# Kernel tuning notes

Measured on AMD Instinct MI355X. Metric: run time of the kernel, lower is better.

## Reference

```python
import jax, jax.numpy as jnp
import numpy as np

B, T, DIM, H = 4, 2048, 512, 8
DECAY = 0.9

def setup_inputs():
    key = jax.random.key(0)
    ks = jax.random.split(key, 8)
    s = 1.0 / np.sqrt(DIM)
    def lin(k):
        return jax.random.normal(k, (DIM, DIM), jnp.float32) * s
    return {
        "q": jax.random.normal(ks[0], (B, T, DIM), jnp.float32),
        "k": jax.random.normal(ks[1], (B, T, DIM), jnp.float32),
        "v": jax.random.normal(ks[2], (B, T, DIM), jnp.float32),
        "Wa": lin(ks[3]), "ba": jnp.zeros((DIM,), jnp.float32),
        "Wb": lin(ks[4]), "bb": jnp.zeros((DIM,), jnp.float32),
        "Wg": lin(ks[5]), "bg": jnp.zeros((DIM,), jnp.float32),
        "Wo": lin(ks[6]), "bo": jnp.zeros((DIM,), jnp.float32),
    }

def _linear_scan(a, b):
    # h_t = a_t * h_{t-1} + b_t along time axis=1, via associative scan
    def combine(c1, c2):
        a1, b1 = c1
        a2, b2 = c2
        return a1 * a2, a2 * b1 + b2
    return jax.lax.associative_scan(combine, (a, b), axis=1)[1]

def reference(q, k, v, Wa, ba, Wb, bb, Wg, bg, Wo, bo):
    # --- Mamba-style selective scan on q (no residual) ---
    a = jax.nn.sigmoid(q @ Wa + ba)   # input-dependent decay [B,T,D]
    b = q @ Wb + bb                   # input injection       [B,T,D]
    h = _linear_scan(a, b)            # recurrent state       [B,T,D]
    g = jax.nn.sigmoid(q @ Wg + bg)   # gate
    m_out = (h * g) @ Wo + bo         # [B,T,D]

    # --- RetNet-style decay-weighted linear retention ---
    Dh = DIM // H
    qh = q.reshape(B, T, H, Dh)
    kh = k.reshape(B, T, H, Dh)
    vh = v.reshape(B, T, H, Dh)
    t = jnp.arange(T)
    delta = t[:, None] - t[None, :]           # t - s
    mask = delta >= 0                         # causal
    decay_mat = jnp.where(
        mask,
        jnp.exp(jnp.where(mask, delta, 0).astype(jnp.float32) * np.float32(np.log(DECAY))),
        0.0,
    )                                          # [T,T]
    scores = jnp.einsum('bthd,bshd->bhts', qh, kh) * decay_mat  # [B,H,T,T]
    r_out = jnp.einsum('bhts,bshd->bthd', scores, vh).reshape(B, T, DIM)

    return m_out + r_out
```

## Files before the change

### kernel.cpp

```cpp
#include <hip/hip_runtime.h>
#include <hip/hip_bf16.h>

typedef unsigned short u16;

#define BB 4
#define TT 2048
#define DIM 512
#define NH 8
#define DH 64
#define DECAY 0.9f

#define CC 64
#define NC 32
#define BHN 32

#define CHS 32
#define NSC 64

#define TM 128
#define TN 128
#define BK 64

#define SS 72

typedef __attribute__((ext_vector_type(8))) short bf16x8;
typedef __attribute__((ext_vector_type(4))) float f32x4;

__device__ __forceinline__ u16 f2bfu(float f) {
  union { float f; unsigned int u; } c; c.f = f;
  unsigned int u = c.u + 0x7FFFu + ((c.u >> 16) & 1u);
  return (u16)(u >> 16);
}
__device__ __forceinline__ float bf2f(u16 u) {
  union { unsigned int u; float f; } c; c.u = ((unsigned int)u) << 16;
  return c.f;
}

__device__ __forceinline__ void gl_lds16(const void* g, void* l) {
  __builtin_amdgcn_global_load_lds(
      (const __attribute__((address_space(1))) void*)g,
      (__attribute__((address_space(3))) void*)(unsigned int)(unsigned long long)l,
      16, 0, 0);
}

__device__ __forceinline__ void gemm_tile(
    int nTile, int mTile, const u16* __restrict__ A, const u16* __restrict__ Bt,
    const float* __restrict__ b0, const float* __restrict__ b1,
    const float* __restrict__ b2,
    u16* __restrict__ C0, u16* __restrict__ C1, u16* __restrict__ C2,
    int act_mask, u16* As, u16* Bs, int tid) {
  int wave = tid >> 6, lane = tid & 63;
  int group = (nTile * TN) >> 9;
  const float* bias = (group == 0) ? b0 : (group == 1) ? b1 : b2;
  u16* C = (group == 0) ? C0 : (group == 1) ? C1 : C2;
  int act = (act_mask >> group) & 1;

  int wm = (wave >> 1) * 64, wn = (wave & 1) * 64;
  int rowA = lane & 15, khalf = lane >> 4;

  f32x4 acc[4][4];
#pragma unroll
  for (int i = 0; i < 4; ++i)
#pragma unroll
    for (int j = 0; j < 4; ++j) acc[i][j] = (f32x4){0.f, 0.f, 0.f, 0.f};

  const u16* Abase = A + (size_t)mTile * TM * 512;
  const u16* Bbase = Bt + (size_t)nTile * TN * 512;

  for (int kk = 0; kk < 512; kk += BK) {
#pragma unroll
    for (int i = 0; i < 4; ++i) {
      int o = (wave * 4 + i) * 64 + lane;
      int row = o >> 3, gk = (o & 7) ^ (row & 7);
      gl_lds16(Abase + (size_t)row * 512 + kk + gk * 8, &As[o * 8]);
    }
#pragma unroll
    for (int i = 0; i < 4; ++i) {
      int o = (wave * 4 + i) * 64 + lane;
      int row = o >> 3, gk = (o & 7) ^ (row & 7);
      gl_lds16(Bbase + (size_t)row * 512 + kk + gk * 8, &Bs[o * 8]);
    }
    __syncthreads();
#pragma unroll
    for (int k0 = 0; k0 < 2; ++k0) {
      bf16x8 af[4], bfr[4];
#pragma unroll
      for (int mi = 0; mi < 4; ++mi) {
        int rr = wm + mi * 16 + rowA;
        int gk = k0 * 4 + khalf;
        int o = rr * 8 + (gk ^ (rr & 7));
        af[mi] = *(const bf16x8*)&As[o * 8];
      }
#pragma unroll
      for (int ni = 0; ni < 4; ++ni) {
        int rr = wn + ni * 16 + rowA;
        int gk = k0 * 4 + khalf;
        int o = rr * 8 + (gk ^ (rr & 7));
        bfr[ni] = *(const bf16x8*)&Bs[o * 8];
      }
#pragma unroll
      for (int mi = 0; mi < 4; ++mi)
#pragma unroll
        for (int ni = 0; ni < 4; ++ni)
          acc[mi][ni] = __builtin_amdgcn_mfma_f32_16x16x32_bf16(
              af[mi], bfr[ni], acc[mi][ni], 0, 0, 0);
    }
    __syncthreads();
  }
  int cloc = lane & 15, rq = (lane >> 4) * 4;
#pragma unroll
  for (int mi = 0; mi < 4; ++mi) {
#pragma unroll
    for (int r = 0; r < 4; ++r) {
      int m = mTile * TM + wm + mi * 16 + rq + r;
#pragma unroll
      for (int ni = 0; ni < 4; ++ni) {
        int n = (nTile * TN + wn + ni * 16 + cloc) & 511;
        float vv = acc[mi][ni][r] + bias[n];
        if (act) vv = 1.0f / (1.0f + __expf(-vv));
        C[(size_t)m * 512 + n] = f2bfu(vv);
      }
    }
  }
}

__device__ __forceinline__ void gemm_tile64(
    int nTile, int mTile, const u16* __restrict__ A, const u16* __restrict__ Bt,
    const float* __restrict__ bias, float* __restrict__ C,
    const u16* __restrict__ Radd, u16* As, u16* Bs, int tid) {
  int wave = tid >> 6, lane = tid & 63;
  int wm = wave * 32;
  int rowA = lane & 15, khalf = lane >> 4;

  f32x4 acc[2][4];
#pragma unroll
  for (int i = 0; i < 2; ++i)
#pragma unroll
    for (int j = 0; j < 4; ++j) acc[i][j] = (f32x4){0.f, 0.f, 0.f, 0.f};

  const u16* Abase = A + (size_t)mTile * TM * 512;
  const u16* Bbase = Bt + (size_t)nTile * 64 * 512;

  for (int kk = 0; kk < 512; kk += BK) {
#pragma unroll
    for (int i = 0; i < 4; ++i) {
      int o = (wave * 4 + i) * 64 + lane;
      int row = o >> 3, gk = (o & 7) ^ (row & 7);
      gl_lds16(Abase + (size_t)row * 512 + kk + gk * 8, &As[o * 8]);
    }
#pragma unroll
    for (int i = 0; i < 2; ++i) {
      int o = (wave * 2 + i) * 64 + lane;
      int row = o >> 3, gk = (o & 7) ^ (row & 7);
      gl_lds16(Bbase + (size_t)row * 512 + kk + gk * 8, &Bs[o * 8]);
    }
    __syncthreads();
#pragma unroll
    for (int k0 = 0; k0 < 2; ++k0) {
      bf16x8 af[2], bfr[4];
#pragma unroll
      for (int mi = 0; mi < 2; ++mi) {
        int rr = wm + mi * 16 + rowA;
        int gk = k0 * 4 + khalf;
        int o = rr * 8 + (gk ^ (rr & 7));
        af[mi] = *(const bf16x8*)&As[o * 8];
      }
#pragma unroll
      for (int ni = 0; ni < 4; ++ni) {
        int rr = ni * 16 + rowA;
        int gk = k0 * 4 + khalf;
        int o = rr * 8 + (gk ^ (rr & 7));
        bfr[ni] = *(const bf16x8*)&Bs[o * 8];
      }
#pragma unroll
      for (int mi = 0; mi < 2; ++mi)
#pragma unroll
        for (int ni = 0; ni < 4; ++ni)
          acc[mi][ni] = __builtin_amdgcn_mfma_f32_16x16x32_bf16(
              af[mi], bfr[ni], acc[mi][ni], 0, 0, 0);
    }
    __syncthreads();
  }
  int cloc = lane & 15, rq = (lane >> 4) * 4;
#pragma unroll
  for (int mi = 0; mi < 2; ++mi) {
#pragma unroll
    for (int r = 0; r < 4; ++r) {
      int m = mTile * TM + wm + mi * 16 + rq + r;
#pragma unroll
      for (int ni = 0; ni < 4; ++ni) {
        int n = nTile * 64 + ni * 16 + cloc;
        float vv = acc[mi][ni][r] + bias[n] + bf2f(Radd[(size_t)m * 512 + n]);
        C[(size_t)m * 512 + n] = vv;
      }
    }
  }
}

__global__ __launch_bounds__(256) void k1_prep_retkv(
    const float* __restrict__ q, u16* __restrict__ qbf,
    const float* __restrict__ W0, const float* __restrict__ W1,
    const float* __restrict__ W2, const float* __restrict__ W3,
    u16* __restrict__ Wt,
    const float* __restrict__ k, const float* __restrict__ v,
    u16* __restrict__ KVTb, u16* __restrict__ VTg) {
  __shared__ __align__(16) u16 smem[2 * 64 * SS];
  __shared__ float t[32][33];
  int bx = blockIdx.x, tid = threadIdx.x;
  if (bx < 1024) {
    int bh = bx & 31, c = bx >> 5;
    int b = bh >> 3, h = bh & 7;
    int wave = tid >> 6, lane = tid & 63;
    u16* VT = smem;
    u16* KT = smem + 64 * SS;
    size_t base = ((size_t)(b * TT + c * CC)) * DIM + h * DH;
    int row = tid >> 2, part = tid & 3, e0 = part * 16;
    float w = __powf(DECAY, (float)(63 - row));
    {
      const float4* vs = (const float4*)(v + base + (size_t)row * DIM + e0);
      const float4* ks = (const float4*)(k + base + (size_t)row * DIM + e0);
#pragma unroll
      for (int u4 = 0; u4 < 4; ++u4) {
        float4 fv = vs[u4], fk = ks[u4];
        VT[(e0 + u4 * 4 + 0) * SS + row] = f2bfu(fv.x);
        VT[(e0 + u4 * 4 + 1) * SS + row] = f2bfu(fv.y);
        VT[(e0 + u4 * 4 + 2) * SS + row] = f2bfu(fv.z);
        VT[(e0 + u4 * 4 + 3) * SS + row] = f2bfu(fv.w);
        KT[(e0 + u4 * 4 + 0) * SS + row] = f2bfu(fk.x * w);
        KT[(e0 + u4 * 4 + 1) * SS + row] = f2bfu(fk.y * w);
        KT[(e0 + u4 * 4 + 2) * SS + row] = f2bfu(fk.z * w);
        KT[(e0 + u4 * 4 + 3) * SS + row] = f2bfu(fk.w * w);
      }
    }
    __syncthreads();
    {
      int e = row;
      u16* dst = VTg + ((size_t)bh * 64 + e) * TT + c * 64 + part * 16;
      *(uint4*)dst = *(const uint4*)&VT[e * SS + part * 16];
      *(uint4*)(dst + 8) = *(const uint4*)&VT[e * SS + part * 16 + 8];
    }
    int wm = (wave >> 1) * 32, wn = (wave & 1) * 32;
    int rowA = lane & 15, khalf = lane >> 4;
    f32x4 acc[2][2];
#pragma unroll
    for (int i = 0; i < 2; ++i)
#pragma unroll
      for (int j = 0; j < 2; ++j) acc[i][j] = (f32x4){0.f, 0.f, 0.f, 0.f};
#pragma unroll
    for (int k0 = 0; k0 < 2; ++k0) {
      int gk = k0 * 4 + khalf;
      bf16x8 af[2], bfr[2];
#pragma unroll
      for (int mi = 0; mi < 2; ++mi)
        af[mi] = *(const bf16x8*)&VT[(wm + mi * 16 + rowA) * SS + gk * 8];
#pragma unroll
      for (int ni = 0; ni < 2; ++ni)
        bfr[ni] = *(const bf16x8*)&KT[(wn + ni * 16 + rowA) * SS + gk * 8];
#pragma unroll
      for (int mi = 0; mi < 2; ++mi)
#pragma unroll
        for (int ni = 0; ni < 2; ++ni)
          acc[mi][ni] = __builtin_amdgcn_mfma_f32_16x16x32_bf16(
              af[mi], bfr[ni], acc[mi][ni], 0, 0, 0);
    }
    int cloc = lane & 15, rq = (lane >> 4) * 4;
    u16* o = KVTb + ((size_t)(c * BHN + bh)) * 4096;
#pragma unroll
    for (int mi = 0; mi < 2; ++mi)
#pragma unroll
      for (int r = 0; r < 4; ++r) {
        int e = wm + mi * 16 + rq + r;
#pragma unroll
        for (int ni = 0; ni < 2; ++ni)
          o[e * 64 + (wn + ni * 16 + cloc)] = f2bfu(acc[mi][ni][r]);
      }
  } else if (bx < 2048) {
    int bx2 = bx - 1024;
    int m = bx2 >> 8, rem = bx2 & 255;
    int n0 = (rem & 15) * 32, k0 = (rem >> 4) * 32;
    const float* W = (m == 0) ? W0 : (m == 1) ? W1 : (m == 2) ? W2 : W3;
    int tx = tid & 31, ty = tid >> 5;
#pragma unroll
    for (int r = 0; r < 32; r += 8)
      t[ty + r][tx] = W[(size_t)(k0 + ty + r) * DIM + n0 + tx];
    __syncthreads();
    u16* o = Wt + (size_t)m * DIM * DIM;
#pragma unroll
    for (int r = 0; r < 32; r += 8)
      o[(size_t)(n0 + ty + r) * DIM + k0 + tx] = f2bfu(t[tx][ty + r]);
  } else {
    int i = (bx - 2048) * 256 + tid;
    float4 f = ((const float4*)q)[i];
    ushort4 u;
    u.x = f2bfu(f.x); u.y = f2bfu(f.y); u.z = f2bfu(f.z); u.w = f2bfu(f.w);
    ((ushort4*)qbf)[i] = u;
  }
}

__global__ __launch_bounds__(256) void k2_gemm1_retscan(
    const u16* __restrict__ qbf, const u16* __restrict__ WtAll,
    const float* __restrict__ ba, const float* __restrict__ bb,
    const float* __restrict__ bg,
    u16* __restrict__ Ab16, u16* __restrict__ Bb16, u16* __restrict__ Gb16,
    const u16* __restrict__ KVTb, u16* __restrict__ Ptb) {
  __shared__ __align__(16) u16 smem[TM * BK + TN * BK];
  int bx = blockIdx.x, tid = threadIdx.x;
  if (bx < 768) {
    int r = bx & 7, t6 = bx >> 3;
    int nT = t6 % 12, s = t6 / 12;
    int mT = (s << 3) | r;
    gemm_tile(nT, mT, qbf, WtAll, ba, bb, bg, Ab16, Bb16, Gb16,
              0b101, smem, smem + TM * BK, tid);
  } else {
    int gid = (bx - 768) * 256 + tid;
    int bh = gid >> 12, ed = gid & 4095;
    float carry = 0.f;
    const float dC = __powf(DECAY, (float)CC);
    for (int c = 0; c < NC; ++c) {
      size_t idx = ((size_t)(c * BHN + bh)) * 4096 + ed;
      Ptb[idx] = f2bfu(carry);
      carry = fmaf(dC, carry, bf2f(KVTb[idx]));
    }
  }
}

__global__ void k3_part(const u16* __restrict__ Ab16, const u16* __restrict__ Bb16,
                        float* __restrict__ SA, float* __restrict__ SB) {
  int ci = blockIdx.x >> 3, grp = blockIdx.x & 7;
  int ch = grp * 256 + threadIdx.x;
  int bb2 = ch >> 9, d = ch & 511;
  size_t base = ((size_t)bb2 * TT + ci * CHS) * DIM + d;
  float h = 0.f, pA = 1.f;
#pragma unroll
  for (int t = 0; t < CHS; ++t) {
    float av = bf2f(Ab16[base + (size_t)t * DIM]);
    float bv = bf2f(Bb16[base + (size_t)t * DIM]);
    h = fmaf(av, h, bv);
    pA *= av;
  }
  SA[ci * 2048 + ch] = pA;
  SB[ci * 2048 + ch] = h;
}

__global__ __launch_bounds__(256) void k4_apply_retout(
    const u16* __restrict__ Ab16, const u16* __restrict__ Bb16,
    const u16* __restrict__ g, const float* __restrict__ SA,
    const float* __restrict__ SB, u16* __restrict__ hg,
    const u16* __restrict__ qbf, const float* __restrict__ kg,
    const u16* __restrict__ VTg, const u16* __restrict__ Ptb,
    u16* __restrict__ routb) {
  __shared__ __align__(16) u16 Sa[64 * SS];
  __shared__ float dp[66];
  int bx = blockIdx.x, tid = threadIdx.x;
  if (bx < 512) {
    int ci = bx >> 3, grp = bx & 7;
    int ch = grp * 256 + tid;
    int bb = ch >> 9, d = ch & 511;
    float carry = 0.f;
    for (int p = 0; p < ci; ++p)
      carry = fmaf(SA[p * 2048 + ch], carry, SB[p * 2048 + ch]);
    size_t base = ((size_t)bb * TT + ci * CHS) * DIM + d;
    float h = carry;
#pragma unroll
    for (int t = 0; t < CHS; ++t) {
      size_t idx = base + (size_t)t * DIM;
      h = fmaf(bf2f(Ab16[idx]), h, bf2f(Bb16[idx]));
      hg[idx] = f2bfu(h * bf2f(g[idx]));
    }
    return;
  }
  int idx2 = bx - 512;
  int bh = idx2 & 31, c = idx2 >> 5;
  int b = bh >> 3, h = bh & 7;
  int wave = tid >> 6, lane = tid & 63;
  size_t base = ((size_t)(b * TT + c * CC)) * DIM + h * DH;
  if (tid < 66) dp[tid] = __powf(DECAY, (float)tid);

  int wm = (wave >> 1) * 32, wn = (wave & 1) * 32;
  int rowA = lane & 15, khalf = lane >> 4;

  bf16x8 afq[2][2];
#pragma unroll
  for (int k0 = 0; k0 < 2; ++k0)
#pragma unroll
    for (int mi = 0; mi < 2; ++mi)
      afq[k0][mi] = *(const bf16x8*)(qbf + base +
          (size_t)(wm + mi * 16 + rowA) * 512 + (k0 * 4 + khalf) * 8);
  bf16x8 bfk[2][2];
#pragma unroll
  for (int k0 = 0; k0 < 2; ++k0)
#pragma unroll
    for (int ni = 0; ni < 2; ++ni) {
      const float* kp = kg + base + (size_t)(wn + ni * 16 + rowA) * 512 +
                        (k0 * 4 + khalf) * 8;
      float4 f0 = *(const float4*)kp;
      float4 f1 = *(const float4*)(kp + 4);
      bf16x8 t;
      t[0] = (short)f2bfu(f0.x); t[1] = (short)f2bfu(f0.y);
      t[2] = (short)f2bfu(f0.z); t[3] = (short)f2bfu(f0.w);
      t[4] = (short)f2bfu(f1.x); t[5] = (short)f2bfu(f1.y);
      t[6] = (short)f2bfu(f1.z); t[7] = (short)f2bfu(f1.w);
      bfk[k0][ni] = t;
    }

  f32x4 accS[2][2];
#pragma unroll
  for (int i = 0; i < 2; ++i)
#pragma unroll
    for (int j = 0; j < 2; ++j) accS[i][j] = (f32x4){0.f, 0.f, 0.f, 0.f};
#pragma unroll
  for (int k0 = 0; k0 < 2; ++k0)
#pragma unroll
    for (int mi = 0; mi < 2; ++mi)
#pragma unroll
      for (int ni = 0; ni < 2; ++ni)
        accS[mi][ni] = __builtin_amdgcn_mfma_f32_16x16x32_bf16(
            afq[k0][mi], bfk[k0][ni], accS[mi][ni], 0, 0, 0);
  __syncthreads();

  int cloc = lane & 15, rq = (lane >> 4) * 4;
#pragma unroll
  for (int mi = 0; mi < 2; ++mi)
#pragma unroll
    for (int ni = 0; ni < 2; ++ni)
#pragma unroll
      for (int r = 0; r < 4; ++r) {
        int i = wm + mi * 16 + rq + r;
        int j = wn + ni * 16 + cloc;
        float sv = (j <= i) ? accS[mi][ni][r] * dp[i - j] : 0.f;
        Sa[i * SS + j] = f2bfu(sv);
      }
#pragma unroll
  for (int mi = 0; mi < 2; ++mi) {
    float s = dp[wm + mi * 16 + rowA + 1];
#pragma unroll
    for (int k0 = 0; k0 < 2; ++k0) {
      bf16x8 t = afq[k0][mi];
#pragma unroll
      for (int u = 0; u < 8; ++u)
        t[u] = (short)f2bfu(bf2f((u16)t[u]) * s);
      afq[k0][mi] = t;
    }
  }
  __syncthreads();

  f32x4 accO[2][2];
#pragma unroll
  for (int i = 0; i < 2; ++i)
#pragma unroll
    for (int j = 0; j < 2; ++j) accO[i][j] = (f32x4){0.f, 0.f, 0.f, 0.f};
#pragma unroll
  for (int k0 = 0; k0 < 4; ++k0) {
    bf16x8 af[2], bfv[2];
#pragma unroll
    for (int mi = 0; mi < 2; ++mi) {
      if (k0 < 2)
        af[mi] = *(const bf16x8*)&Sa[(wm + mi * 16 + rowA) * SS +
                                     (k0 * 4 + khalf) * 8];
      else
        af[mi] = afq[k0 - 2][mi];
    }
#pragma unroll
    for (int ni = 0; ni < 2; ++ni) {
      int e = wn + ni * 16 + rowA;
      if (k0 < 2)
        bfv[ni] = *(const bf16x8*)(VTg + ((size_t)bh * 64 + e) * TT + c * 64 +
                                   (k0 * 4 + khalf) * 8);
      else
        bfv[ni] = *(const bf16x8*)(Ptb + ((size_t)(c * BHN + bh)) * 4096 +
                                   e * 64 + ((k0 - 2) * 4 + khalf) * 8);
    }
#pragma unroll
    for (int mi = 0; mi < 2; ++mi)
#pragma unroll
      for (int ni = 0; ni < 2; ++ni)
        accO[mi][ni] = __builtin_amdgcn_mfma_f32_16x16x32_bf16(
            af[mi], bfv[ni], accO[mi][ni], 0, 0, 0);
  }
#pragma unroll
  for (int mi = 0; mi < 2; ++mi)
#pragma unroll
    for (int r = 0; r < 4; ++r) {
      int i = wm + mi * 16 + rq + r;
#pragma unroll
      for (int ni = 0; ni < 2; ++ni) {
        int e = wn + ni * 16 + cloc;
        routb[base + (size_t)i * 512 + e] = f2bfu(accO[mi][ni][r]);
      }
    }
}

__global__ __launch_bounds__(256) void k5_gemm2(
    const u16* __restrict__ hgbf, const u16* __restrict__ Wto,
    const float* __restrict__ bo, float* __restrict__ out,
    const u16* __restrict__ routb) {
  __shared__ __align__(16) u16 smem[TM * BK + 64 * BK];
  int bx = blockIdx.x;
  int r = bx & 7, t6 = bx >> 3;
  int nT = t6 & 7, s = t6 >> 3;
  int mT = (s << 3) | r;
  gemm_tile64(nT, mT, hgbf, Wto, bo, out, routb,
              smem, smem + TM * BK, threadIdx.x);
}

extern "C" void kernel_launch(void* const* d_in, const int* in_sizes, int n_in,
                              void* d_out, int out_size, void* d_ws, size_t ws_size,
                              hipStream_t stream) {
  const float* q  = (const float*)d_in[0];
  const float* k  = (const float*)d_in[1];
  const float* v  = (const float*)d_in[2];
  const float* Wa = (const float*)d_in[3];
  const float* ba = (const float*)d_in[4];
  const float* Wb = (const float*)d_in[5];
  const float* bb = (const float*)d_in[6];
  const float* Wg = (const float*)d_in[7];
  const float* bg = (const float*)d_in[8];
  const float* Wo = (const float*)d_in[9];
  const float* bo = (const float*)d_in[10];
  float* out = (float*)d_out;
  float* ws = (float*)d_ws;

  const size_t NEL = (size_t)BB * TT * DIM;
  float* SA = ws;
  float* SB = SA + NSC * 2048;
  u16* up = (u16*)(SB + NSC * 2048);
  u16* Ab16  = up;  up += NEL;
  u16* Bb16  = up;  up += NEL;
  u16* Gb16  = up;  up += NEL;
  u16* qbf   = up;  up += NEL;
  u16* hgbf  = up;  up += NEL;
  u16* WtAll = up;  up += 4 * DIM * DIM;
  u16* KVTb  = up;  up += (size_t)NC * BHN * 4096;
  u16* Ptb   = up;  up += (size_t)NC * BHN * 4096;
  u16* VTg   = up;  up += (size_t)BHN * 64 * TT;
  u16* routb = up;  up += NEL;

  k1_prep_retkv<<<6144, 256, 0, stream>>>(q, qbf, Wa, Wb, Wg, Wo, WtAll,
                                          k, v, KVTb, VTg);

  k2_gemm1_retscan<<<1280, 256, 0, stream>>>(qbf, WtAll, ba, bb, bg,
                                             Ab16, Bb16, Gb16, KVTb, Ptb);

  k3_part<<<512, 256, 0, stream>>>(Ab16, Bb16, SA, SB);

  k4_apply_retout<<<1536, 256, 0, stream>>>(Ab16, Bb16, Gb16, SA, SB, hgbf,
                                            qbf, k, VTg, Ptb, routb);

  k5_gemm2<<<512, 256, 0, stream>>>(hgbf, WtAll + 3 * DIM * DIM,
                                    bo, out, routb);
}
```

Baseline: 173.0 us.

## Fuse retention output with scan partials and reuse prescaled bf16 K chunks

The retention intra-chunk block now runs alongside the Mamba chunk-partial scan in one launch, and the Mamba apply pass becomes a separate small kernel afterwards. This reshuffles which work overlaps with the serial carry loop. K is also stored once in k1 as decay-prescaled bf16 in a chunk-contiguous layout, so the retention kernel loads it directly instead of reading and converting fp32 k. The diagonal decay becomes a per-row factor (dpi[i], from the prescaled K) rather than a per-pair lookup. The cost is an extra workspace buffer and extra writes in k1, plus possible precision differences from prescaling K by up to 0.9^-63 weights before the bf16 rounding.

```diff
diff --git a/kernel.cpp b/kernel.cpp
--- a/kernel.cpp
+++ b/kernel.cpp
@@ -203,7 +203,7 @@
     const float* __restrict__ W2, const float* __restrict__ W3,
     u16* __restrict__ Wt,
     const float* __restrict__ k, const float* __restrict__ v,
-    u16* __restrict__ KVTb, u16* __restrict__ VTg) {
+    u16* __restrict__ KVTb, u16* __restrict__ VTg, u16* __restrict__ kcb) {
   __shared__ __align__(16) u16 smem[2 * 64 * SS];
   __shared__ float t[32][33];
   int bx = blockIdx.x, tid = threadIdx.x;
@@ -216,6 +216,7 @@
     size_t base = ((size_t)(b * TT + c * CC)) * DIM + h * DH;
     int row = tid >> 2, part = tid & 3, e0 = part * 16;
     float w = __powf(DECAY, (float)(63 - row));
+    __align__(16) u16 krow[16];
     {
       const float4* vs = (const float4*)(v + base + (size_t)row * DIM + e0);
       const float4* ks = (const float4*)(k + base + (size_t)row * DIM + e0);
@@ -226,11 +227,20 @@
         VT[(e0 + u4 * 4 + 1) * SS + row] = f2bfu(fv.y);
         VT[(e0 + u4 * 4 + 2) * SS + row] = f2bfu(fv.z);
         VT[(e0 + u4 * 4 + 3) * SS + row] = f2bfu(fv.w);
-        KT[(e0 + u4 * 4 + 0) * SS + row] = f2bfu(fk.x * w);
-        KT[(e0 + u4 * 4 + 1) * SS + row] = f2bfu(fk.y * w);
-        KT[(e0 + u4 * 4 + 2) * SS + row] = f2bfu(fk.z * w);
-        KT[(e0 + u4 * 4 + 3) * SS + row] = f2bfu(fk.w * w);
-      }
+        u16 k0s = f2bfu(fk.x * w), k1s = f2bfu(fk.y * w);
+        u16 k2s = f2bfu(fk.z * w), k3s = f2bfu(fk.w * w);
+        KT[(e0 + u4 * 4 + 0) * SS + row] = k0s;
+        KT[(e0 + u4 * 4 + 1) * SS + row] = k1s;
+        KT[(e0 + u4 * 4 + 2) * SS + row] = k2s;
+        KT[(e0 + u4 * 4 + 3) * SS + row] = k3s;
+        krow[u4 * 4 + 0] = k0s; krow[u4 * 4 + 1] = k1s;
+        krow[u4 * 4 + 2] = k2s; krow[u4 * 4 + 3] = k3s;
+      }
+    }
+    {
+      u16* kdst = kcb + (((size_t)bh * NC + c) * 64 + row) * 64 + e0;
+      *(uint4*)kdst = *(const uint4*)&krow[0];
+      *(uint4*)(kdst + 8) = *(const uint4*)&krow[8];
     }
     __syncthreads();
     {
@@ -324,57 +334,40 @@
   }
 }
 
-__global__ void k3_part(const u16* __restrict__ Ab16, const u16* __restrict__ Bb16,
-                        float* __restrict__ SA, float* __restrict__ SB) {
-  int ci = blockIdx.x >> 3, grp = blockIdx.x & 7;
-  int ch = grp * 256 + threadIdx.x;
-  int bb2 = ch >> 9, d = ch & 511;
-  size_t base = ((size_t)bb2 * TT + ci * CHS) * DIM + d;
-  float h = 0.f, pA = 1.f;
-#pragma unroll
-  for (int t = 0; t < CHS; ++t) {
-    float av = bf2f(Ab16[base + (size_t)t * DIM]);
-    float bv = bf2f(Bb16[base + (size_t)t * DIM]);
-    h = fmaf(av, h, bv);
-    pA *= av;
-  }
-  SA[ci * 2048 + ch] = pA;
-  SB[ci * 2048 + ch] = h;
-}
-
-__global__ __launch_bounds__(256) void k4_apply_retout(
+__global__ __launch_bounds__(256) void k3_retout_part(
     const u16* __restrict__ Ab16, const u16* __restrict__ Bb16,
-    const u16* __restrict__ g, const float* __restrict__ SA,
-    const float* __restrict__ SB, u16* __restrict__ hg,
-    const u16* __restrict__ qbf, const float* __restrict__ kg,
+    float* __restrict__ SA, float* __restrict__ SB,
+    const u16* __restrict__ qbf, const u16* __restrict__ kcb,
     const u16* __restrict__ VTg, const u16* __restrict__ Ptb,
     u16* __restrict__ routb) {
   __shared__ __align__(16) u16 Sa[64 * SS];
   __shared__ float dp[66];
+  __shared__ float dpi[64];
   int bx = blockIdx.x, tid = threadIdx.x;
-  if (bx < 512) {
-    int ci = bx >> 3, grp = bx & 7;
+  if (bx >= 1024) {
+    int bxp = bx - 1024;
+    int ci = bxp >> 3, grp = bxp & 7;
     int ch = grp * 256 + tid;
-    int bb = ch >> 9, d = ch & 511;
-    float carry = 0.f;
-    for (int p = 0; p < ci; ++p)
-      carry = fmaf(SA[p * 2048 + ch], carry, SB[p * 2048 + ch]);
-    size_t base = ((size_t)bb * TT + ci * CHS) * DIM + d;
-    float h = carry;
+    int bb2 = ch >> 9, d = ch & 511;
+    size_t base = ((size_t)bb2 * TT + ci * CHS) * DIM + d;
+    float h = 0.f, pA = 1.f;
 #pragma unroll
     for (int t = 0; t < CHS; ++t) {
-      size_t idx = base + (size_t)t * DIM;
-      h = fmaf(bf2f(Ab16[idx]), h, bf2f(Bb16[idx]));
-      hg[idx] = f2bfu(h * bf2f(g[idx]));
-    }
+      float av = bf2f(Ab16[base + (size_t)t * DIM]);
+      float bv = bf2f(Bb16[base + (size_t)t * DIM]);
+      h = fmaf(av, h, bv);
+      pA *= av;
+    }
+    SA[ci * 2048 + ch] = pA;
+    SB[ci * 2048 + ch] = h;
     return;
   }
-  int idx2 = bx - 512;
-  int bh = idx2 & 31, c = idx2 >> 5;
+  int bh = bx & 31, c = bx >> 5;
   int b = bh >> 3, h = bh & 7;
   int wave = tid >> 6, lane = tid & 63;
   size_t base = ((size_t)(b * TT + c * CC)) * DIM + h * DH;
   if (tid < 66) dp[tid] = __powf(DECAY, (float)tid);
+  if (tid < 64) dpi[tid] = __powf(DECAY, (float)tid - 63.0f);
 
   int wm = (wave >> 1) * 32, wn = (wave & 1) * 32;
   int rowA = lane & 15, khalf = lane >> 4;
@@ -386,22 +379,14 @@
     for (int mi = 0; mi < 2; ++mi)
       afq[k0][mi] = *(const bf16x8*)(qbf + base +
           (size_t)(wm + mi * 16 + rowA) * 512 + (k0 * 4 + khalf) * 8);
+  const u16* kcbase = kcb + ((size_t)bh * NC + c) * 64 * 64;
   bf16x8 bfk[2][2];
 #pragma unroll
   for (int k0 = 0; k0 < 2; ++k0)
 #pragma unroll
-    for (int ni = 0; ni < 2; ++ni) {
-      const float* kp = kg + base + (size_t)(wn + ni * 16 + rowA) * 512 +
-                        (k0 * 4 + khalf) * 8;
-      float4 f0 = *(const float4*)kp;
-      float4 f1 = *(const float4*)(kp + 4);
-      bf16x8 t;
-      t[0] = (short)f2bfu(f0.x); t[1] = (short)f2bfu(f0.y);
-      t[2] = (short)f2bfu(f0.z); t[3] = (short)f2bfu(f0.w);
-      t[4] = (short)f2bfu(f1.x); t[5] = (short)f2bfu(f1.y);
-      t[6] = (short)f2bfu(f1.z); t[7] = (short)f2bfu(f1.w);
-      bfk[k0][ni] = t;
-    }
+    for (int ni = 0; ni < 2; ++ni)
+      bfk[k0][ni] = *(const bf16x8*)(kcbase +
+          (size_t)(wn + ni * 16 + rowA) * 64 + (k0 * 4 + khalf) * 8);
 
   f32x4 accS[2][2];
 #pragma unroll
@@ -427,7 +412,7 @@
       for (int r = 0; r < 4; ++r) {
         int i = wm + mi * 16 + rq + r;
         int j = wn + ni * 16 + cloc;
-        float sv = (j <= i) ? accS[mi][ni][r] * dp[i - j] : 0.f;
+        float sv = (j <= i) ? accS[mi][ni][r] * dpi[i] : 0.f;
         Sa[i * SS + j] = f2bfu(sv);
       }
 #pragma unroll
@@ -488,6 +473,27 @@
         routb[base + (size_t)i * 512 + e] = f2bfu(accO[mi][ni][r]);
       }
     }
+}
+
+__global__ __launch_bounds__(256) void k4_apply(
+    const u16* __restrict__ Ab16, const u16* __restrict__ Bb16,
+    const u16* __restrict__ g, const float* __restrict__ SA,
+    const float* __restrict__ SB, u16* __restrict__ hg) {
+  int bx = blockIdx.x, tid = threadIdx.x;
+  int ci = bx >> 3, grp = bx & 7;
+  int ch = grp * 256 + tid;
+  int bb = ch >> 9, d = ch & 511;
+  float carry = 0.f;
+  for (int p = 0; p < ci; ++p)
+    carry = fmaf(SA[p * 2048 + ch], carry, SB[p * 2048 + ch]);
+  size_t base = ((size_t)bb * TT + ci * CHS) * DIM + d;
+  float h = carry;
+#pragma unroll
+  for (int t = 0; t < CHS; ++t) {
+    size_t idx = base + (size_t)t * DIM;
+    h = fmaf(bf2f(Ab16[idx]), h, bf2f(Bb16[idx]));
+    hg[idx] = f2bfu(h * bf2f(g[idx]));
+  }
 }
 
 __global__ __launch_bounds__(256) void k5_gemm2(
@@ -534,17 +540,18 @@
   u16* Ptb   = up;  up += (size_t)NC * BHN * 4096;
   u16* VTg   = up;  up += (size_t)BHN * 64 * TT;
   u16* routb = up;  up += NEL;
+  u16* kcb   = up;  up += (size_t)BHN * NC * 64 * 64;
 
   k1_prep_retkv<<<6144, 256, 0, stream>>>(q, qbf, Wa, Wb, Wg, Wo, WtAll,
-                                          k, v, KVTb, VTg);
+                                          k, v, KVTb, VTg, kcb);
 
   k2_gemm1_retscan<<<1280, 256, 0, stream>>>(qbf, WtAll, ba, bb, bg,
                                              Ab16, Bb16, Gb16, KVTb, Ptb);
 
-  k3_part<<<512, 256, 0, stream>>>(Ab16, Bb16, SA, SB);
-
-  k4_apply_retout<<<1536, 256, 0, stream>>>(Ab16, Bb16, Gb16, SA, SB, hgbf,
-                                            qbf, k, VTg, Ptb, routb);
+  k3_retout_part<<<1536, 256, 0, stream>>>(Ab16, Bb16, SA, SB,
+                                           qbf, kcb, VTg, Ptb, routb);
+
+  k4_apply<<<512, 256, 0, stream>>>(Ab16, Bb16, Gb16, SA, SB, hgbf);
 
   k5_gemm2<<<512, 256, 0, stream>>>(hgbf, WtAll + 3 * DIM * DIM,
                                     bo, out, routb);
```

Result: no change. 174.4 us (+0.8%).
